# Optimization experiments

Measured on AMD Instinct MI355X. Metric: run time of the kernel, lower is better.

## Reference

```python
import jax, jax.numpy as jnp
import numpy as np

B, H, K, D = 4096, 512, 32, 20


def setup_inputs() -> dict:
    key = jax.random.key(0)
    k1, k2 = jax.random.split(key)
    hidden = jax.random.normal(k1, (B, H), dtype=jnp.float32)
    # cluster: soft assignment probabilities (rows sum to 1), like a softmax output
    c = jax.random.uniform(k2, (B, K), dtype=jnp.float32)
    cluster = c / jnp.sum(c, axis=-1, keepdims=True)
    return {"hidden": hidden, "cluster": cluster, "d": D}


def reference(hidden, cluster, d):
    # softHidden[b,h,k] = hidden[b,h] * cluster[b,k]
    soft_hidden = hidden[:, :, None] * cluster[:, None, :]          # [B,H,K]
    class_sums = jnp.sum(soft_hidden, axis=0)                        # [H,K] (code calls these "class_means" but they are sums)
    within = jnp.sum((soft_hidden - class_sums[None]) ** 2, axis=0)  # [H,K]
    # round() has zero gradient in torch; mirror that with stop_gradient
    counts = jax.lax.stop_gradient(jnp.round(jnp.sum(cluster, axis=0)))  # [K]

    m = class_sums.T   # [K,H]
    w = within.T       # [K,H]

    # all class pairs i<j (the nested Python loops, vectorized)
    i, j = jnp.triu_indices(K, k=1)   # each [P], P = K*(K-1)/2
    mi, mj = m[i], m[j]                               # [P,H]
    gm = (mi + mj) / 2.0
    between = (mi - gm) ** 2 * counts[i][:, None] + (mj - gm) ** 2 * counts[j][:, None]
    pair_within = w[i] + w[j]                         # [P,H]
    pair_count = counts[i] + counts[j]                # [P]

    d2 = pair_count - 2.0
    d2 = jnp.where(d2 == 0.0, d2 + 1e-5, d2)
    x = between / (between + pair_within)
    x = jnp.clip(x, 1e-37, 1.0 - 1e-5)
    # regularized incomplete beta I_x(d1/2, d2/2) with d1 = 1
    xbetainc = jax.scipy.special.betainc(0.5, (d2 / 2.0)[:, None], x)  # [P,H]

    top_k, _ = jax.lax.top_k(xbetainc, d)             # [P,d]
    per_pair = jnp.sum(jnp.log(top_k), axis=-1)       # [P]
    return -jnp.sum(per_pair)
```

## Files before the change

### kernel.cpp

```cpp
#include <hip/hip_runtime.h>
#include <math.h>

#define BB 4096
#define HH 512
#define KK 32
#define PAIRS ((KK * (KK - 1)) / 2)

constexpr int TH  = 16;
constexpr int NBB = 16;
constexpr int BC  = BB / NBB;
constexpr int SUB = 64;
constexpr int GK  = 16;
constexpr int RP  = 17;


struct TabE {
    float v[2048];
    constexpr TabE() : v{} {
        double c = 1.0; v[0] = 1.0f;
        for (int j = 1; j < 2048; ++j) { c *= (2.0*j - 1.0) / (2.0*j); v[j] = (float)c; }
    }
};
struct TabO {
    float v[2048];
    constexpr TabO() : v{} {
        double c = 1.0; v[0] = 1.0f;
        for (int j = 1; j < 2048; ++j) { c *= (2.0*j) / (2.0*j + 1.0); v[j] = (float)c; }
    }
};
__device__ constexpr TabE tab_e{};
__device__ constexpr TabO tab_o{};

__global__ __launch_bounds__(256) void stage1_kernel(
    const float* __restrict__ hidden, const float* __restrict__ cluster,
    float* __restrict__ part_m, float* __restrict__ part_s,
    float* __restrict__ pcol, float* __restrict__ ctl)
{
    __shared__ float hid_s[SUB * TH];
    __shared__ float clu_s[SUB * KK];
    __shared__ float red  [GK * KK * RP];
    __shared__ float cred [GK * KK];

    const int t  = threadIdx.x;
    const int g  = t >> 4;
    const int tx = t & 15;
    const int h0 = blockIdx.x * TH;
    const int c  = blockIdx.y;
    const int bchunk = c * BC;

    if (blockIdx.x == 0 && c == 0 && t == 0) {
        ctl[0] = 0.0f;
        ((unsigned*)ctl)[1] = 0u;
    }

    float am0[TH], am1[TH], as0[TH], as1[TH];
#pragma unroll
    for (int i = 0; i < TH; ++i) { am0[i]=0.f; am1[i]=0.f; as0[i]=0.f; as1[i]=0.f; }
    float cs0 = 0.f, cs1 = 0.f;

    const float4* hid4 = (const float4*)hidden;
    const float4* clu4 = (const float4*)cluster;

    for (int sub = 0; sub < BC; sub += SUB) {
        const int b0 = bchunk + sub;
        {
            int r = t >> 2, q = t & 3;
            ((float4*)hid_s)[t] =
                hid4[(size_t)(b0 + r) * (HH / 4) + (h0 >> 2) + q];
        }
#pragma unroll
        for (int e = 0; e < 2; ++e) {
            int u = t + e * 256;
            int r = u >> 3, q = u & 7;
            ((float4*)clu_s)[u] = clu4[(size_t)(b0 + r) * (KK / 4) + q];
        }
        __syncthreads();

        const float4* h4 = (const float4*)hid_s;
#pragma unroll
        for (int s = 0; s < SUB / GK; ++s) {
            int r = s * GK + g;
            float c0 = clu_s[r * KK + tx];
            float c1 = clu_s[r * KK + tx + 16];
            cs0 += c0; cs1 += c1;
            float c0q = c0 * c0, c1q = c1 * c1;
            float4 a0 = h4[r*4+0], a1 = h4[r*4+1], a2 = h4[r*4+2], a3 = h4[r*4+3];
#define DO_H(idx, val)                                              \
            { float v_ = (val); float vq_ = v_ * v_;                \
              am0[idx] = fmaf(v_,  c0,  am0[idx]);                  \
              am1[idx] = fmaf(v_,  c1,  am1[idx]);                  \
              as0[idx] = fmaf(vq_, c0q, as0[idx]);                  \
              as1[idx] = fmaf(vq_, c1q, as1[idx]); }
            DO_H(0,  a0.x) DO_H(1,  a0.y) DO_H(2,  a0.z) DO_H(3,  a0.w)
            DO_H(4,  a1.x) DO_H(5,  a1.y) DO_H(6,  a1.z) DO_H(7,  a1.w)
            DO_H(8,  a2.x) DO_H(9,  a2.y) DO_H(10, a2.z) DO_H(11, a2.w)
            DO_H(12, a3.x) DO_H(13, a3.y) DO_H(14, a3.z) DO_H(15, a3.w)
#undef DO_H
        }
        __syncthreads();
    }

    cred[g * KK + tx]      = cs0;
    cred[g * KK + tx + 16] = cs1;
    __syncthreads();
    if (blockIdx.x == 0 && t < KK) {
        float v = 0.f;
#pragma unroll
        for (int g2 = 0; g2 < GK; ++g2) v += cred[g2 * KK + t];
        pcol[c * KK + t] = v;
    }

#pragma unroll
    for (int h = 0; h < TH; ++h) {
        red[(g * KK + tx)      * RP + h] = am0[h];
        red[(g * KK + tx + 16) * RP + h] = am1[h];
    }
    __syncthreads();
#pragma unroll
    for (int e = 0; e < 2; ++e) {
        int u = t + e * 256;
        int k = u >> 4, h = u & 15;
        float v = 0.f;
#pragma unroll
        for (int g2 = 0; g2 < GK; ++g2) v += red[(g2 * KK + k) * RP + h];
        part_m[((size_t)c * KK + k) * HH + h0 + h] = v;
    }
    __syncthreads();
#pragma unroll
    for (int h = 0; h < TH; ++h) {
        red[(g * KK + tx)      * RP + h] = as0[h];
        red[(g * KK + tx + 16) * RP + h] = as1[h];
    }
    __syncthreads();
#pragma unroll
    for (int e = 0; e < 2; ++e) {
        int u = t + e * 256;
        int k = u >> 4, h = u & 15;
        float v = 0.f;
#pragma unroll
        for (int g2 = 0; g2 < GK; ++g2) v += red[(g2 * KK + k) * RP + h];
        part_s[((size_t)c * KK + k) * HH + h0 + h] = v;
    }
}

__device__ __forceinline__ float frcp(float x) {
#if __has_builtin(__builtin_amdgcn_rcpf)
    return __builtin_amdgcn_rcpf(x);
#else
    return 1.0f / x;
#endif
}
__device__ __forceinline__ float guardf(float t) {
    return (fabsf(t) < 1e-30f) ? 1e-30f : t;
}

__device__ float betacf_fast(float a, float b, float x)
{
    const float EPS = 1e-5f;
    float qab = a + b, qap = a + 1.0f, qam = a - 1.0f;
    float c = 1.0f;
    float d = frcp(guardf(1.0f - qab * x * frcp(qap)));
    float h = d;
    for (int m = 1; m <= 100; ++m) {
        float fm = (float)m, m2 = 2.0f * fm;
        float aa = fm * (b - fm) * x * frcp((qam + m2) * (a + m2));
        d = frcp(guardf(fmaf(aa, d, 1.0f)));
        c = guardf(fmaf(aa, frcp(c), 1.0f));
        h *= d * c;
        float aa2 = -(a + fm) * (qab + fm) * x * frcp((a + m2) * (qap + m2));
        d = frcp(guardf(fmaf(aa2, d, 1.0f)));
        c = guardf(fmaf(aa2, frcp(c), 1.0f));
        float del = d * c;
        h *= del;
        if (__all(fabsf(del - 1.0f) < EPS)) break;
    }
    return h;
}

__global__ __launch_bounds__(256) void stage2_kernel(
    const float* __restrict__ part_m, const float* __restrict__ part_s,
    const float* __restrict__ pcol, float* __restrict__ ctl,
    const int* __restrict__ dptr, float* __restrict__ out)
{
    __shared__ float xs[HH];

    const int t = threadIdx.x;
    const int w = t >> 6, lane = t & 63;
    const int p = blockIdx.x;

    int i = 0, rem = p;
    while (true) { int row = KK - 1 - i; if (rem < row) break; rem -= row; ++i; }
    const int j = i + 1 + rem;

    float ci = 0.f, cj = 0.f;
#pragma unroll
    for (int cc = 0; cc < NBB; ++cc) {
        ci += pcol[cc * KK + i];
        cj += pcol[cc * KK + j];
    }
    ci = roundf(ci); cj = roundf(cj);
    const float pc = ci + cj;
    float d2 = pc - 2.0f;
    if (d2 == 0.0f) d2 = 1e-5f;
    const float b = 0.5f * d2;

#pragma unroll
    for (int q = 0; q < 2; ++q) {
        int h = w * 128 + q * 64 + lane;
        float mi = 0.f, mj = 0.f, si = 0.f, sj = 0.f;
#pragma unroll
        for (int cc = 0; cc < NBB; ++cc) {
            size_t base = (size_t)cc * KK * HH;
            mi += part_m[base + (size_t)i * HH + h];
            mj += part_m[base + (size_t)j * HH + h];
            si += part_s[base + (size_t)i * HH + h];
            sj += part_s[base + (size_t)j * HH + h];
        }
        float wi = fmaf((float)(BB - 2) * mi, mi, si);
        float wj = fmaf((float)(BB - 2) * mj, mj, sj);
        float dm = 0.5f * (mi - mj);
        float between = dm * dm * pc;
        float denom = between + wi + wj;
        float x = between / denom;
        if (!(x >= 1e-37f)) x = 1e-37f;
        x = fminf(x, 1.0f - 1e-5f);
        xs[h] = x;
    }
    __syncthreads();
    if (w != 0) return;

    float lv[8];
#pragma unroll
    for (int q = 0; q < 8; ++q) lv[q] = xs[q * 64 + lane];

    const int d = *dptr;
    float myx = 0.004f;
    float lm = lv[0];
#pragma unroll
    for (int q = 1; q < 8; ++q) lm = fmaxf(lm, lv[q]);

    for (int r = 0; r < d; ++r) {
        float gm = lm;
#pragma unroll
        for (int off = 1; off < 64; off <<= 1)
            gm = fmaxf(gm, __shfl_xor(gm, off));
        unsigned long long msk = __ballot(lm == gm);
        int winner = __ffsll((unsigned long long)msk) - 1;
        if (lane == r) myx = gm;
        if (lane == winner) {
            bool done = false;
#pragma unroll
            for (int q = 0; q < 8; ++q)
                if (!done && lv[q] == gm) { lv[q] = -1.0f; done = true; }
            lm = lv[0];
#pragma unroll
            for (int q = 1; q < 8; ++q) lm = fmaxf(lm, lv[q]);
        }
    }

    float x  = myx;
    float u  = 1.0f - x;
    float sx = sqrtf(x);
    int nu = (int)(d2 + 0.5f);
    float L;
    if (nu >= 1 && nu <= 4094 && fabsf(d2 - (float)nu) < 1e-3f) {
        float u2 = u * u;
        if (nu & 1) {
            int terms = (nu - 1) >> 1;
            float S = 0.f;
            if (terms > 0) {
                float S0 = 0.f, S1 = 0.f, p0 = 1.f, p1 = u;
                int jj = 0;
                for (; jj + 1 < terms; jj += 2) {
                    S0 = fmaf(tab_o.v[jj],     p0, S0);
                    S1 = fmaf(tab_o.v[jj + 1], p1, S1);
                    p0 *= u2; p1 *= u2;
                }
                if (jj < terms) S0 = fmaf(tab_o.v[jj], p0, S0);
                S = S0 + S1;
            }
            float theta = asinf(fminf(sx, 1.0f));
            float A = 0.636619772367581343f * (theta + sx * sqrtf(u) * S);
            L = logf(fminf(A, 1.0f));
        } else {
            int terms = nu >> 1;
            float S0 = 0.f, S1 = 0.f, p0 = 1.f, p1 = u;
            int jj = 0;
            for (; jj + 1 < terms; jj += 2) {
                S0 = fmaf(tab_e.v[jj],     p0, S0);
                S1 = fmaf(tab_e.v[jj + 1], p1, S1);
                p0 *= u2; p1 *= u2;
            }
            if (jj < terms) S0 = fmaf(tab_e.v[jj], p0, S0);
            float A = sx * (S0 + S1);
            L = logf(fminf(A, 1.0f));
        }
    } else {
        const float a = 0.5f;
        const float lg = lgammaf(a + b) - lgammaf(b) - 0.57236494f;
        const float xsplit = (a + 1.0f) / (a + b + 2.0f);
        bool  brA = x < xsplit;
        float al  = brA ? a : b;
        float be  = brA ? b : a;
        float xx  = brA ? x : u;
        float cf  = betacf_fast(al, be, xx);
        float lbt = lg + 0.5f * logf(x) + b * logf(u);
        if (brA) {
            L = lbt + logf(2.0f * fmaxf(cf, 1e-30f));
        } else {
            float tt = expf(lbt) * cf / b;
            tt = fminf(tt, 0.99999988f);
            L = log1pf(-tt);
        }
    }

    float val = (lane < d) ? L : 0.0f;
#pragma unroll
    for (int off = 1; off < 64; off <<= 1) val += __shfl_xor(val, off);

    if (lane == 0) {
        atomicAdd(&ctl[0], -val);
        __threadfence();
        unsigned old = atomicAdd((unsigned*)ctl + 1, 1u);
        if (old == PAIRS - 1) {
            out[0] = atomicAdd(&ctl[0], 0.0f);
        }
    }
}

extern "C" void kernel_launch(void* const* d_in, const int* in_sizes, int n_in,
                              void* d_out, int out_size, void* d_ws, size_t ws_size,
                              hipStream_t stream)
{
    const float* hidden  = (const float*)d_in[0];
    const float* cluster = (const float*)d_in[1];
    const int*   dptr    = (const int*)d_in[2];

    float* part_m = (float*)d_ws;
    float* part_s = part_m + (size_t)NBB * KK * HH;
    float* pcol   = part_s + (size_t)NBB * KK * HH;
    float* ctl    = pcol + NBB * KK;

    dim3 g1(HH / TH, NBB);
    stage1_kernel<<<g1, 256, 0, stream>>>(hidden, cluster,
                                          part_m, part_s, pcol, ctl);
    stage2_kernel<<<PAIRS, 256, 0, stream>>>(part_m, part_s, pcol, ctl,
                                             dptr, (float*)d_out);
}
```

Measured before the change: 95.42 us.

## Add separate reduction kernel for partial sums and shrink stage2 to one wave

Moves the reduction of per-chunk partial sums and column counts into a dedicated reduce kernel, so each class's sum and within value is computed once. Before, every one of the 496 pair blocks re-summed 16 partials for two classes. Stage2 now runs one 64-thread wave per pair that reads the precomputed sums directly, with no shared-memory staging or block barrier. The cost is an extra kernel launch and an extra global round trip for the reduced arrays, and the control-word reset moves into the new kernel.

```diff
diff --git a/kernel.cpp b/kernel.cpp
--- a/kernel.cpp
+++ b/kernel.cpp
@@ -34,7 +34,7 @@
 __global__ __launch_bounds__(256) void stage1_kernel(
     const float* __restrict__ hidden, const float* __restrict__ cluster,
     float* __restrict__ part_m, float* __restrict__ part_s,
-    float* __restrict__ pcol, float* __restrict__ ctl)
+    float* __restrict__ pcol)
 {
     __shared__ float hid_s[SUB * TH];
     __shared__ float clu_s[SUB * KK];
@@ -47,11 +47,6 @@
     const int h0 = blockIdx.x * TH;
     const int c  = blockIdx.y;
     const int bchunk = c * BC;
-
-    if (blockIdx.x == 0 && c == 0 && t == 0) {
-        ctl[0] = 0.0f;
-        ((unsigned*)ctl)[1] = 0u;
-    }
 
     float am0[TH], am1[TH], as0[TH], as1[TH];
 #pragma unroll
@@ -143,6 +138,48 @@
     }
 }
 
+__global__ __launch_bounds__(256) void reduce_kernel(
+    const float* __restrict__ part_m, const float* __restrict__ part_s,
+    const float* __restrict__ pcol,
+    float* __restrict__ msum, float* __restrict__ wsum,
+    float* __restrict__ counts, float* __restrict__ ctl)
+{
+    const int t = threadIdx.x;
+    const int g = blockIdx.x * 256 + t;
+    const size_t idx = (size_t)g;
+    const size_t cstride = (size_t)KK * HH / 4;
+
+    const float4* pm4 = (const float4*)part_m;
+    const float4* ps4 = (const float4*)part_s;
+
+    float4 m = make_float4(0.f, 0.f, 0.f, 0.f);
+    float4 s = make_float4(0.f, 0.f, 0.f, 0.f);
+#pragma unroll
+    for (int cc = 0; cc < NBB; ++cc) {
+        float4 a = pm4[cc * cstride + idx];
+        float4 b = ps4[cc * cstride + idx];
+        m.x += a.x; m.y += a.y; m.z += a.z; m.w += a.w;
+        s.x += b.x; s.y += b.y; s.z += b.z; s.w += b.w;
+    }
+    float4 w;
+    w.x = fmaf((float)(BB - 2) * m.x, m.x, s.x);
+    w.y = fmaf((float)(BB - 2) * m.y, m.y, s.y);
+    w.z = fmaf((float)(BB - 2) * m.z, m.z, s.z);
+    w.w = fmaf((float)(BB - 2) * m.w, m.w, s.w);
+    ((float4*)msum)[g] = m;
+    ((float4*)wsum)[g] = w;
+
+    if (blockIdx.x == 0) {
+        if (t < KK) {
+            float v = 0.f;
+#pragma unroll
+            for (int cc = 0; cc < NBB; ++cc) v += pcol[cc * KK + t];
+            counts[t] = roundf(v);
+        }
+        if (t == 0) { ctl[0] = 0.0f; ((unsigned*)ctl)[1] = 0u; }
+    }
+}
+
 __device__ __forceinline__ float frcp(float x) {
 #if __has_builtin(__builtin_amdgcn_rcpf)
     return __builtin_amdgcn_rcpf(x);
@@ -177,61 +214,44 @@
     return h;
 }
 
-__global__ __launch_bounds__(256) void stage2_kernel(
-    const float* __restrict__ part_m, const float* __restrict__ part_s,
-    const float* __restrict__ pcol, float* __restrict__ ctl,
+__global__ __launch_bounds__(64) void stage2_kernel(
+    const float* __restrict__ msum, const float* __restrict__ wsum,
+    const float* __restrict__ counts, float* __restrict__ ctl,
     const int* __restrict__ dptr, float* __restrict__ out)
 {
-    __shared__ float xs[HH];
-
-    const int t = threadIdx.x;
-    const int w = t >> 6, lane = t & 63;
+    const int lane = threadIdx.x;
     const int p = blockIdx.x;
 
     int i = 0, rem = p;
     while (true) { int row = KK - 1 - i; if (rem < row) break; rem -= row; ++i; }
     const int j = i + 1 + rem;
 
-    float ci = 0.f, cj = 0.f;
-#pragma unroll
-    for (int cc = 0; cc < NBB; ++cc) {
-        ci += pcol[cc * KK + i];
-        cj += pcol[cc * KK + j];
-    }
-    ci = roundf(ci); cj = roundf(cj);
+    const float ci = counts[i];
+    const float cj = counts[j];
     const float pc = ci + cj;
     float d2 = pc - 2.0f;
     if (d2 == 0.0f) d2 = 1e-5f;
     const float b = 0.5f * d2;
 
-#pragma unroll
-    for (int q = 0; q < 2; ++q) {
-        int h = w * 128 + q * 64 + lane;
-        float mi = 0.f, mj = 0.f, si = 0.f, sj = 0.f;
-#pragma unroll
-        for (int cc = 0; cc < NBB; ++cc) {
-            size_t base = (size_t)cc * KK * HH;
-            mi += part_m[base + (size_t)i * HH + h];
-            mj += part_m[base + (size_t)j * HH + h];
-            si += part_s[base + (size_t)i * HH + h];
-            sj += part_s[base + (size_t)j * HH + h];
-        }
-        float wi = fmaf((float)(BB - 2) * mi, mi, si);
-        float wj = fmaf((float)(BB - 2) * mj, mj, sj);
+    const float* mi_p = msum + (size_t)i * HH;
+    const float* mj_p = msum + (size_t)j * HH;
+    const float* wi_p = wsum + (size_t)i * HH;
+    const float* wj_p = wsum + (size_t)j * HH;
+
+    float lv[8];
+#pragma unroll
+    for (int q = 0; q < 8; ++q) {
+        int h = q * 64 + lane;
+        float mi = mi_p[h], mj = mj_p[h];
+        float wi = wi_p[h], wj = wj_p[h];
         float dm = 0.5f * (mi - mj);
         float between = dm * dm * pc;
         float denom = between + wi + wj;
         float x = between / denom;
         if (!(x >= 1e-37f)) x = 1e-37f;
         x = fminf(x, 1.0f - 1e-5f);
-        xs[h] = x;
-    }
-    __syncthreads();
-    if (w != 0) return;
-
-    float lv[8];
-#pragma unroll
-    for (int q = 0; q < 8; ++q) lv[q] = xs[q * 64 + lane];
+        lv[q] = x;
+    }
 
     const int d = *dptr;
     float myx = 0.004f;
@@ -339,11 +359,16 @@
     float* part_m = (float*)d_ws;
     float* part_s = part_m + (size_t)NBB * KK * HH;
     float* pcol   = part_s + (size_t)NBB * KK * HH;
-    float* ctl    = pcol + NBB * KK;
+    float* msum   = pcol + NBB * KK;
+    float* wsum   = msum + KK * HH;
+    float* counts = wsum + KK * HH;
+    float* ctl    = counts + KK;
 
     dim3 g1(HH / TH, NBB);
     stage1_kernel<<<g1, 256, 0, stream>>>(hidden, cluster,
-                                          part_m, part_s, pcol, ctl);
-    stage2_kernel<<<PAIRS, 256, 0, stream>>>(part_m, part_s, pcol, ctl,
-                                             dptr, (float*)d_out);
-}
+                                          part_m, part_s, pcol);
+    reduce_kernel<<<KK * HH / 4 / 256, 256, 0, stream>>>(part_m, part_s, pcol,
+                                                         msum, wsum, counts, ctl);
+    stage2_kernel<<<PAIRS, 64, 0, stream>>>(msum, wsum, counts, ctl,
+                                            dptr, (float*)d_out);
+}
```

After: 96.13 us. About the same (+0.7%).
